# Performance work log

Hardware: AMD Instinct MI355X
Metric: run time of the kernel (lower is better)

The kernel has to match this reference:

```python
import jax, jax.numpy as jnp
import numpy as np

B, N, D, E, H = 4, 2048, 512, 16, 1024
CAP = max(4, min(N, int(N * 2.0 / E)))   # eval capacity_factor = 2.0 -> 256
EPS = 1e-9
THRESH = 0.2  # second_threshold_eval


def setup_inputs() -> dict:
    key = jax.random.key(0)
    ks = jax.random.split(key, 10)
    f32 = jnp.float32
    return {
        "X": jax.random.normal(ks[0], (B, N, D), f32),
        "probs": jax.random.uniform(ks[1], (B, N), f32),
        "W1": jax.random.normal(ks[2], (D, D), f32) * (1.0 / np.sqrt(D)),
        "b1": jnp.zeros((D,), f32),
        "Wg": jax.random.normal(ks[3], (D, E), f32),  # Top2Gating uses randn init
        "We1": jax.random.normal(ks[4], (E, D, H), f32) * (1.0 / np.sqrt(D)),
        "We2": jax.random.normal(ks[5], (E, H, D), f32) * (1.0 / np.sqrt(H)),
        "W3": jax.random.normal(ks[6], (D, 4), f32) * (1.0 / np.sqrt(D)),
        "b3": jnp.zeros((4,), f32),
        "W4": jax.random.normal(ks[7], (4, 1), f32) * 0.5,
        "b4": jnp.zeros((1,), f32),
    }


def top2_gating(x, Wg, probs):
    # x: [B, N, D] -> raw gates [B, N, E]
    raw = jax.nn.softmax(jnp.einsum('bnd,de->bne', x, Wg), axis=-1)
    dt = raw.dtype

    gate1 = jnp.max(raw, axis=-1)
    idx1 = jnp.argmax(raw, axis=-1)
    mask1 = jax.nn.one_hot(idx1, E, dtype=dt)
    density_proxy = raw

    raw_wo1 = raw * (1.0 - mask1)
    gate2 = jnp.max(raw_wo1, axis=-1)
    idx2 = jnp.argmax(raw_wo1, axis=-1)
    mask2 = jax.nn.one_hot(idx2, E, dtype=dt)

    denom = gate1 + gate2 + EPS
    gate1 = gate1 / denom
    gate2 = gate2 / denom

    # load-balancing loss (computed but wrapper discards it)
    density1 = jnp.mean(mask1, axis=-2)
    loss = jnp.mean(jnp.mean(density_proxy, axis=-2) * density1) * float(E ** 2)

    # second policy == 'random'
    mask2 = mask2 * (probs < (gate2 / max(THRESH, EPS))).astype(dt)[..., None]

    # exclusive cumsum along the group dim gives position within each expert
    pos1 = (jnp.cumsum(mask1, axis=-2) - mask1) * mask1          # [B, N, E]
    mask1 = mask1 * (pos1 < float(CAP)).astype(dt)
    mask1_count = jnp.sum(mask1, axis=-2, keepdims=True)
    mask1_flat = jnp.sum(mask1, axis=-1)                          # [B, N]
    pos1_flat = jnp.sum(pos1, axis=-1)
    gate1 = gate1 * mask1_flat

    pos2 = ((jnp.cumsum(mask2, axis=-2) - mask2) + mask1_count) * mask2
    mask2 = mask2 * (pos2 < float(CAP)).astype(dt)
    mask2_flat = jnp.sum(mask2, axis=-1)
    pos2_flat = jnp.sum(pos2, axis=-1)
    gate2 = gate2 * mask2_flat

    # safe one-hot: out-of-range positions map to all-zeros (jax.nn.one_hot semantics)
    oh_p1 = jax.nn.one_hot(pos1_flat.astype(jnp.int32), CAP, dtype=dt)
    oh_p2 = jax.nn.one_hot(pos2_flat.astype(jnp.int32), CAP, dtype=dt)
    oh_e1 = jax.nn.one_hot(idx1, E, dtype=dt)
    oh_e2 = jax.nn.one_hot(idx2, E, dtype=dt)

    combine = ((gate1 * mask1_flat)[..., None, None] * oh_e1[..., :, None] * oh_p1[..., None, :]
               + (gate2 * mask2_flat)[..., None, None] * oh_e2[..., :, None] * oh_p2[..., None, :])
    dispatch = (combine != 0).astype(dt)
    return dispatch, combine, loss


def reference(X, probs, W1, b1, Wg, We1, We2, W3, b3, W4, b4):
    h = X @ W1 + b1                                              # linear1
    dispatch, combine, loss = top2_gating(h, Wg, probs)
    exp_in = jnp.einsum('bnd,bnec->ebcd', h, dispatch)           # dispatch
    hid = jax.nn.leaky_relu(jnp.einsum('ebcd,edh->ebch', exp_in, We1))
    exp_out = jnp.einsum('ebch,ehd->ebcd', hid, We2)             # experts
    moe_out = jnp.einsum('bnec,ebcd->bnd', combine, exp_out)     # combine
    out = (moe_out @ W3 + b3) @ W4 + b4                          # hidden3 -> act3
    return out
```

## Files before the change

kernel.cpp:

```cpp
#include <hip/hip_runtime.h>
#include <hip/hip_bf16.h>

#define NB 4
#define NN 2048
#define ND 512
#define NE 16
#define NH 1024
#define CAP 256
#define NTOK (NB*NN)

typedef __attribute__((ext_vector_type(8))) short bf16x8;
typedef __attribute__((ext_vector_type(4))) float f32x4;
typedef __attribute__((ext_vector_type(8))) unsigned short u16x8;

__device__ __forceinline__ void gload16(const void* gsrc, void* lds) {
    __builtin_amdgcn_global_load_lds((const __attribute__((address_space(1))) void*)gsrc,
                                     (__attribute__((address_space(3))) void*)lds, 16, 0, 0);
}
__device__ __forceinline__ unsigned short f2bf(float f) {
    union { __hip_bfloat16 b; unsigned short u; } v; v.b = __float2bfloat16(f); return v.u;
}

__global__ __launch_bounds__(256) void prep_kernel(const float* __restrict__ W1,
                                                   const float* __restrict__ Wg,
                                                   const float* __restrict__ We1,
                                                   const float* __restrict__ We2,
                                                   const float* __restrict__ W3,
                                                   const float* __restrict__ W4,
                                                   unsigned short* __restrict__ W1B,
                                                   unsigned short* __restrict__ We1B,
                                                   float* __restrict__ WcT,
                                                   float* __restrict__ u,
                                                   float* __restrict__ zbuf) {
    const int tid = threadIdx.x;
    int bid = blockIdx.x;
    if (bid < 512) {
        __shared__ float vvs[ND];
        {
            int d = tid * 2;
            float s0 = 0.f, s1 = 0.f;
            #pragma unroll
            for (int j = 0; j < 4; ++j) {
                s0 += W3[d * 4 + j] * W4[j];
                s1 += W3[(d + 1) * 4 + j] * W4[j];
            }
            vvs[d] = s0; vvs[d + 1] = s1;
        }
        if (bid == 0) zbuf[tid] = 0.f;
        __syncthreads();
        const int w = tid >> 6, l = tid & 63;
        const float4* vv4 = (const float4*)vvs;
        const float4 v0 = vv4[l], v1 = vv4[l + 64];
        float sums[8];
        #pragma unroll
        for (int i = 0; i < 8; ++i) {
            int gr = bid * 32 + w * 8 + i;
            const float4* row = (const float4*)(We2 + (size_t)gr * ND);
            float4 a0 = row[l], a1 = row[l + 64];
            sums[i] = a0.x * v0.x + a0.y * v0.y + a0.z * v0.z + a0.w * v0.w
                    + a1.x * v1.x + a1.y * v1.y + a1.z * v1.z + a1.w * v1.w;
        }
        #pragma unroll
        for (int off = 32; off >= 1; off >>= 1)
            #pragma unroll
            for (int i = 0; i < 8; ++i) sums[i] += __shfl_xor(sums[i], off);
        if (l == 0) {
            int gr0 = bid * 32 + w * 8;
            #pragma unroll
            for (int i = 0; i < 8; ++i) u[gr0 + i] = sums[i];
        }
        return;
    }
    bid -= 512;
    if (bid < 128) {
        const int w = tid >> 6, l = tid & 63;
        const int d = bid * 4 + w;
        float a0 = 0.f, a1 = 0.f, a2 = 0.f, a3 = 0.f, a4 = 0.f, a5 = 0.f, a6 = 0.f, a7 = 0.f;
        float a8 = 0.f, a9 = 0.f, aA = 0.f, aB = 0.f, aC = 0.f, aD = 0.f, aE = 0.f, aF = 0.f;
        #pragma unroll
        for (int ch = 0; ch < 8; ++ch) {
            float x = W1[(size_t)d * ND + ch * 64 + l];
            const float4* wg4 = (const float4*)(Wg + (size_t)(ch * 64 + l) * NE);
            float4 g0 = wg4[0], g1 = wg4[1], g2 = wg4[2], g3 = wg4[3];
            a0 = fmaf(x, g0.x, a0); a1 = fmaf(x, g0.y, a1); a2 = fmaf(x, g0.z, a2); a3 = fmaf(x, g0.w, a3);
            a4 = fmaf(x, g1.x, a4); a5 = fmaf(x, g1.y, a5); a6 = fmaf(x, g1.z, a6); a7 = fmaf(x, g1.w, a7);
            a8 = fmaf(x, g2.x, a8); a9 = fmaf(x, g2.y, a9); aA = fmaf(x, g2.z, aA); aB = fmaf(x, g2.w, aB);
            aC = fmaf(x, g3.x, aC); aD = fmaf(x, g3.y, aD); aE = fmaf(x, g3.z, aE); aF = fmaf(x, g3.w, aF);
        }
        float accs[16] = {a0, a1, a2, a3, a4, a5, a6, a7, a8, a9, aA, aB, aC, aD, aE, aF};
        #pragma unroll
        for (int off = 32; off >= 1; off >>= 1)
            #pragma unroll
            for (int e = 0; e < 16; ++e) accs[e] += __shfl_xor(accs[e], off);
        #pragma unroll
        for (int e = 0; e < 16; ++e)
            if (l == e) WcT[e * ND + d] = accs[e];
        return;
    }
    bid -= 128;
    {
        const float* src; unsigned short* dst; int C; size_t so, dof;
        int d0;
        if (bid < 16) {
            int dblk = bid >> 1, hblk = bid & 1;
            src = W1; C = ND; so = 0;
            d0 = dblk * 64;
            dof = (size_t)(dblk * 512 + hblk * 256) * 64;
            dst = W1B + dof + (size_t)tid * 64;
            src += (size_t)d0 * C + hblk * 256 + tid;
        } else {
            int tb = bid - 16;
            int e = tb >> 5, rem = tb & 31;
            int dblk = rem >> 2, hblk = rem & 3;
            src = We1; C = NH;
            so = (size_t)e * ND * NH;
            d0 = dblk * 64;
            dof = (size_t)((e * 8 + dblk) * NH + hblk * 256) * 64;
            dst = We1B + dof + (size_t)tid * 64;
            src += so + (size_t)d0 * C + hblk * 256 + tid;
        }
        float v[64];
        #pragma unroll
        for (int j = 0; j < 64; ++j) v[j] = src[(size_t)j * C];
        #pragma unroll
        for (int q = 0; q < 8; ++q) {
            u16x8 o;
            #pragma unroll
            for (int j = 0; j < 8; ++j) o[j] = f2bf(v[q * 8 + j]);
            *(u16x8*)(dst + q * 8) = o;
        }
    }
}

__global__ __launch_bounds__(256) void gating_kernel(const float* __restrict__ X,
                                                     const float* __restrict__ WcT,
                                                     const float* __restrict__ probs,
                                                     unsigned short* __restrict__ Xbf,
                                                     int* __restrict__ idx1a, int* __restrict__ idx2a,
                                                     float* __restrict__ g1a, float* __restrict__ g2a,
                                                     int* __restrict__ pos1a, int* __restrict__ pos2a) {
    __shared__ float wc[NE * ND];
    const int tid = threadIdx.x;
    #pragma unroll
    for (int i = 0; i < 32; ++i) wc[tid + 256 * i] = WcT[tid + 256 * i];
    __syncthreads();
    const int w = tid >> 6, l = tid & 63;
    const float4* wc4 = (const float4*)wc;
    for (int j = 0; j < 4; ++j) {
        int tok = blockIdx.x * 16 + j * 4 + w;
        const float4* xrow = (const float4*)(X + (size_t)tok * ND);
        float4 x0 = xrow[l], x1 = xrow[l + 64];
        {
            ushort4 o0, o1;
            o0.x = f2bf(x0.x); o0.y = f2bf(x0.y); o0.z = f2bf(x0.z); o0.w = f2bf(x0.w);
            o1.x = f2bf(x1.x); o1.y = f2bf(x1.y); o1.z = f2bf(x1.z); o1.w = f2bf(x1.w);
            *(ushort4*)(Xbf + (size_t)tok * ND + 4 * l) = o0;
            *(ushort4*)(Xbf + (size_t)tok * ND + 256 + 4 * l) = o1;
        }
        float acc[NE];
        #pragma unroll
        for (int e = 0; e < NE; ++e) {
            float4 w0 = wc4[e * 128 + l], w1 = wc4[e * 128 + l + 64];
            acc[e] = x0.x * w0.x + x0.y * w0.y + x0.z * w0.z + x0.w * w0.w
                   + x1.x * w1.x + x1.y * w1.y + x1.z * w1.z + x1.w * w1.w;
        }
        #pragma unroll
        for (int off = 32; off >= 1; off >>= 1)
            #pragma unroll
            for (int e = 0; e < NE; ++e) acc[e] += __shfl_xor(acc[e], off);

        if (l == 0) {
            float m = acc[0];
            #pragma unroll
            for (int e = 1; e < NE; ++e) m = fmaxf(m, acc[e]);
            float raw[NE]; float s = 0.f;
            #pragma unroll
            for (int e = 0; e < NE; ++e) { raw[e] = expf(acc[e] - m); s += raw[e]; }
            #pragma unroll
            for (int e = 0; e < NE; ++e) raw[e] = raw[e] / s;
            int i1 = 0; float g1 = raw[0];
            #pragma unroll
            for (int e = 1; e < NE; ++e) if (raw[e] > g1) { g1 = raw[e]; i1 = e; }
            int i2 = -1; float g2 = -1.f;
            #pragma unroll
            for (int e = 0; e < NE; ++e) if (e != i1 && raw[e] > g2) { g2 = raw[e]; i2 = e; }
            float denom = g1 + g2 + 1e-9f;
            float g1n = g1 / denom, g2n = g2 / denom;
            bool flag = probs[tok] < (g2n / 0.2f);
            idx1a[tok] = i1;
            idx2a[tok] = flag ? i2 : -1;
            g1a[tok] = g1n;
            g2a[tok] = g2n;
            pos1a[tok] = -1;
            pos2a[tok] = -1;
        }
    }
}

__global__ __launch_bounds__(512) void scan_linear1_kernel(const int* __restrict__ idx1a,
                                                           const int* __restrict__ idx2a,
                                                           int* __restrict__ pos1a, int* __restrict__ pos2a,
                                                           int* __restrict__ slot_token,
                                                           const unsigned short* __restrict__ Xbf,
                                                           const unsigned short* __restrict__ W1B,
                                                           const float* __restrict__ b1,
                                                           unsigned short* __restrict__ hbf) {
    __shared__ char smem[65536];
    const int tid = threadIdx.x;
    const int w = tid >> 6, l = tid & 63;
    if (blockIdx.x < 64) {
        const int bb = blockIdx.x;
        const int b = bb >> 4, e = bb & 15;
        int* cnt1 = (int*)smem;
        int* cnt2 = cnt1 + 8;
        int* slot = slot_token + (e * NB + b) * CAP;
        const unsigned long long below = (l == 0) ? 0ull : ((1ull << l) - 1ull);
        const int base0 = w * 256;
        int c1 = 0, c2 = 0;
        #pragma unroll
        for (int it = 0; it < 4; ++it) {
            int n = base0 + it * 64 + l;
            c1 += __popcll(__ballot(idx1a[b * NN + n] == e));
            c2 += __popcll(__ballot(idx2a[b * NN + n] == e));
        }
        if (l == 0) { cnt1[w] = c1; cnt2[w] = c2; }
        __syncthreads();
        int b1c = 0, t1 = 0, b2c = 0, t2 = 0;
        #pragma unroll
        for (int i = 0; i < 8; ++i) {
            int v1 = cnt1[i], v2 = cnt2[i];
            if (i < w) { b1c += v1; b2c += v2; }
            t1 += v1; t2 += v2;
        }
        const int start2 = (t1 < CAP) ? t1 : CAP;
        int c = b1c;
        #pragma unroll
        for (int it = 0; it < 4; ++it) {
            int n = base0 + it * 64 + l;
            bool p = (idx1a[b * NN + n] == e);
            unsigned long long m = __ballot(p);
            int pre = __popcll(m & below);
            if (p) { int pos = c + pre; if (pos < CAP) { slot[pos] = n; pos1a[b * NN + n] = pos; } }
            c += __popcll(m);
        }
        c = start2 + b2c;
        #pragma unroll
        for (int it = 0; it < 4; ++it) {
            int n = base0 + it * 64 + l;
            bool p = (idx2a[b * NN + n] == e);
            unsigned long long m = __ballot(p);
            int pre = __popcll(m & below);
            if (p) { int pos = c + pre; if (pos < CAP) { slot[pos] = n; pos2a[b * NN + n] = pos; } }
            c += __popcll(m);
        }
        int nfill = start2 + t2; nfill = (nfill < CAP) ? nfill : CAP;
        for (int i = nfill + tid; i < CAP; i += 512) slot[i] = -1;
        return;
    }
    const int lb = blockIdx.x - 64;
    const int m0 = (lb >> 2) * 128, n0 = (lb & 3) * 128;
    const int wm = w >> 1, wn = w & 1;
    const int lr = l & 15, lk = l >> 4;
    char* Ash0 = smem;
    char* Bsh0 = smem + 32768;

    auto stage = [&](int Ks, int buf) {
        #pragma unroll
        for (int i = 0; i < 2; ++i) {
            int o = i * 8192 + tid * 16;
            int r = o >> 7, bb = o & 127;
            int sb = bb ^ ((r & 7) << 4);
            gload16((const char*)Xbf + ((size_t)(m0 + r) * ND + Ks * 64) * 2 + sb,
                    Ash0 + buf * 16384 + i * 8192 + w * 1024);
            gload16((const char*)W1B + ((size_t)(Ks * 512 + n0 + r) * 64) * 2 + sb,
                    Bsh0 + buf * 16384 + i * 8192 + w * 1024);
        }
    };

    f32x4 acc[2][4] = {};
    stage(0, 0);
    __syncthreads();
    for (int Ks = 0; Ks < 8; ++Ks) {
        int buf = Ks & 1;
        if (Ks < 7) stage(Ks + 1, buf ^ 1);
        #pragma unroll
        for (int k32 = 0; k32 < 2; ++k32) {
            int kb = (k32 * 32 + 8 * lk) * 2;
            bf16x8 a[2], bfr[4];
            #pragma unroll
            for (int mi = 0; mi < 2; ++mi) {
                int row = wm * 32 + mi * 16 + lr;
                a[mi] = *(const bf16x8*)(Ash0 + buf * 16384 + row * 128 + (kb ^ ((row & 7) << 4)));
            }
            #pragma unroll
            for (int ni = 0; ni < 4; ++ni) {
                int row = wn * 64 + ni * 16 + lr;
                bfr[ni] = *(const bf16x8*)(Bsh0 + buf * 16384 + row * 128 + (kb ^ ((row & 7) << 4)));
            }
            #pragma unroll
            for (int mi = 0; mi < 2; ++mi)
                #pragma unroll
                for (int ni = 0; ni < 4; ++ni)
                    acc[mi][ni] = __builtin_amdgcn_mfma_f32_16x16x32_bf16(a[mi], bfr[ni], acc[mi][ni], 0, 0, 0);
        }
        __syncthreads();
    }
    #pragma unroll
    for (int mi = 0; mi < 2; ++mi)
        #pragma unroll
        for (int ni = 0; ni < 4; ++ni) {
            int col = n0 + wn * 64 + ni * 16 + lr;
            float bb1 = b1[col];
            #pragma unroll
            for (int r = 0; r < 4; ++r) {
                int m = m0 + wm * 32 + mi * 16 + lk * 4 + r;
                hbf[(size_t)m * ND + col] = f2bf(acc[mi][ni][r] + bb1);
            }
        }
}

__global__ __launch_bounds__(512) void expert_mfma_kernel(const unsigned short* __restrict__ hbf,
                                                          const unsigned short* __restrict__ We1B,
                                                          const float* __restrict__ u,
                                                          const int* __restrict__ slot_token,
                                                          const float* __restrict__ zbuf,
                                                          float* __restrict__ s_slot) {
    __shared__ char Ash[65536];
    __shared__ char Bsh[2][32768];
    __shared__ float u_lds[NH];
    __shared__ float sbuf[8][32];
    __shared__ int toks[64];
    const int tid = threadIdx.x;
    const int w = tid >> 6, l = tid & 63;
    const int wm = w >> 2, wn = w & 3;
    const int lr = l & 15, lk = l >> 4;
    const int bid = blockIdx.x;
    const int e = (bid & 7) | ((bid >> 7) << 3);
    const int chunk = (bid >> 3) & 15;
    const int b = chunk >> 2, c0 = (chunk & 3) * 64;

    if (tid < 64) toks[tid] = slot_token[(e * NB + b) * CAP + c0 + tid];
    u_lds[tid] = u[e * NH + tid];
    u_lds[tid + 512] = u[e * NH + tid + 512];
    __syncthreads();
    #pragma unroll
    for (int i = 0; i < 8; ++i) {
        int r = i * 8 + w;
        int t = toks[r];
        int sb = (l * 16) ^ ((r & 7) << 4);
        const char* src = (t >= 0) ? ((const char*)hbf + ((size_t)(b * NN + t) * ND) * 2 + sb)
                                   : ((const char*)zbuf + sb);
        gload16(src, Ash + i * 8192 + w * 1024);
    }
    auto stageB = [&](int s, int buf) {
        int Hc = s >> 3, Ks = s & 7;
        #pragma unroll
        for (int i = 0; i < 4; ++i) {
            int o = i * 8192 + tid * 16;
            int r = o >> 7, bb = o & 127;
            int sb = bb ^ ((r & 7) << 4);
            gload16((const char*)We1B + (((size_t)(e * 8 + Ks) * NH + Hc * 256 + r) * 64) * 2 + sb,
                    Bsh[buf] + i * 8192 + w * 1024);
        }
    };
    f32x4 acc[2][4] = {};
    float srow[2][4] = {};
    stageB(0, 0);
    __syncthreads();
    for (int s = 0; s < 32; ++s) {
        int buf = s & 1;
        if (s < 31) stageB(s + 1, buf ^ 1);
        #pragma unroll
        for (int k32 = 0; k32 < 2; ++k32) {
            int kbA = ((s & 7) * 64 + k32 * 32 + 8 * lk) * 2;
            int kbB = (k32 * 32 + 8 * lk) * 2;
            bf16x8 a[2], bfr[4];
            #pragma unroll
            for (int mi = 0; mi < 2; ++mi) {
                int row = wm * 32 + mi * 16 + lr;
                a[mi] = *(const bf16x8*)(Ash + row * 1024 + (kbA ^ ((row & 7) << 4)));
            }
            #pragma unroll
            for (int ni = 0; ni < 4; ++ni) {
                int row = wn * 64 + ni * 16 + lr;
                bfr[ni] = *(const bf16x8*)(Bsh[buf] + row * 128 + (kbB ^ ((row & 7) << 4)));
            }
            #pragma unroll
            for (int mi = 0; mi < 2; ++mi)
                #pragma unroll
                for (int ni = 0; ni < 4; ++ni)
                    acc[mi][ni] = __builtin_amdgcn_mfma_f32_16x16x32_bf16(a[mi], bfr[ni], acc[mi][ni], 0, 0, 0);
        }
        if ((s & 7) == 7) {
            int Hc = s >> 3;
            #pragma unroll
            for (int mi = 0; mi < 2; ++mi)
                #pragma unroll
                for (int ni = 0; ni < 4; ++ni) {
                    float uu = u_lds[Hc * 256 + wn * 64 + ni * 16 + lr];
                    #pragma unroll
                    for (int r = 0; r < 4; ++r) {
                        float x = acc[mi][ni][r];
                        x = (x > 0.f) ? x : 0.01f * x;
                        srow[mi][r] = fmaf(x, uu, srow[mi][r]);
                        acc[mi][ni][r] = 0.f;
                    }
                }
        }
        __syncthreads();
    }
    #pragma unroll
    for (int off = 1; off < 16; off <<= 1)
        #pragma unroll
        for (int mi = 0; mi < 2; ++mi)
            #pragma unroll
            for (int r = 0; r < 4; ++r)
                srow[mi][r] += __shfl_xor(srow[mi][r], off);
    if (lr == 0) {
        #pragma unroll
        for (int mi = 0; mi < 2; ++mi)
            #pragma unroll
            for (int r = 0; r < 4; ++r)
                sbuf[w][mi * 16 + lk * 4 + r] = srow[mi][r];
    }
    __syncthreads();
    if (tid < 64) {
        int q = tid >> 5, rl = tid & 31;
        float s = sbuf[q * 4 + 0][rl] + sbuf[q * 4 + 1][rl] + sbuf[q * 4 + 2][rl] + sbuf[q * 4 + 3][rl];
        s_slot[(e * NB + b) * CAP + c0 + tid] = s;
    }
}

__global__ __launch_bounds__(256) void final_kernel(const int* __restrict__ idx1a, const int* __restrict__ idx2a,
                                                    const int* __restrict__ pos1a, const int* __restrict__ pos2a,
                                                    const float* __restrict__ g1a, const float* __restrict__ g2a,
                                                    const float* __restrict__ s_slot,
                                                    const float* __restrict__ b3, const float* __restrict__ W4,
                                                    const float* __restrict__ b4,
                                                    float* __restrict__ out) {
    int tok = blockIdx.x * 256 + threadIdx.x;
    int b = tok >> 11;
    float c0v = 0.f;
    #pragma unroll
    for (int j = 0; j < 4; ++j) c0v += b3[j] * W4[j];
    float s = c0v + b4[0];
    int p1 = pos1a[tok];
    if (p1 >= 0) s += g1a[tok] * s_slot[(idx1a[tok] * NB + b) * CAP + p1];
    int p2 = pos2a[tok];
    if (p2 >= 0) s += g2a[tok] * s_slot[(idx2a[tok] * NB + b) * CAP + p2];
    out[tok] = s;
}

extern "C" void kernel_launch(void* const* d_in, const int* in_sizes, int n_in,
                              void* d_out, int out_size, void* d_ws, size_t ws_size,
                              hipStream_t stream) {
    const float* X    = (const float*)d_in[0];
    const float* probs= (const float*)d_in[1];
    const float* W1   = (const float*)d_in[2];
    const float* b1   = (const float*)d_in[3];
    const float* Wg   = (const float*)d_in[4];
    const float* We1  = (const float*)d_in[5];
    const float* We2  = (const float*)d_in[6];
    const float* W3   = (const float*)d_in[7];
    const float* b3   = (const float*)d_in[8];
    const float* W4   = (const float*)d_in[9];
    const float* b4   = (const float*)d_in[10];
    float* out = (float*)d_out;

    char* ws = (char*)d_ws;
    size_t off = 0;
    auto alloc = [&](size_t bytes) { void* p = ws + off; off += (bytes + 255) & ~(size_t)255; return p; };
    unsigned short* Xbf  = (unsigned short*)alloc((size_t)NTOK * ND * 2);
    unsigned short* hbf  = (unsigned short*)alloc((size_t)NTOK * ND * 2);
    unsigned short* W1B  = (unsigned short*)alloc((size_t)ND * ND * 2);
    unsigned short* We1B = (unsigned short*)alloc((size_t)NE * NH * ND * 2);
    float* WcT     = (float*)alloc(NE * ND * 4);
    float* u       = (float*)alloc(NE * NH * 4);
    float* zbuf    = (float*)alloc(1024);
    int*   idx1a   = (int*)alloc(NTOK * 4);
    int*   idx2a   = (int*)alloc(NTOK * 4);
    int*   pos1a   = (int*)alloc(NTOK * 4);
    int*   pos2a   = (int*)alloc(NTOK * 4);
    float* g1a     = (float*)alloc(NTOK * 4);
    float* g2a     = (float*)alloc(NTOK * 4);
    int*   slot_tok= (int*)alloc(NE * NB * CAP * 4);
    float* s_slot  = (float*)alloc(NE * NB * CAP * 4);
    (void)ws_size; (void)in_sizes; (void)n_in; (void)out_size;

    prep_kernel<<<1168, 256, 0, stream>>>(W1, Wg, We1, We2, W3, W4,
                                          W1B, We1B, WcT, u, zbuf);
    gating_kernel<<<NTOK / 16, 256, 0, stream>>>(X, WcT, probs, Xbf,
                                                 idx1a, idx2a, g1a, g2a, pos1a, pos2a);
    scan_linear1_kernel<<<64 + 256, 512, 0, stream>>>(idx1a, idx2a, pos1a, pos2a, slot_tok,
                                                      Xbf, W1B, b1, hbf);
    expert_mfma_kernel<<<256, 512, 0, stream>>>(hbf, We1B, u, slot_tok, zbuf, s_slot);
    final_kernel<<<NTOK / 256, 256, 0, stream>>>(idx1a, idx2a, pos1a, pos2a, g1a, g2a, s_slot, b3, W4, b4, out);
}
```

Measured before the change: 90.06 us.

## Move We1 bf16 conversion and We2 projection into scan/linear1 kernel

The expert-weight preprocessing (converting We1 to bf16 tiles and projecting We2 onto W3·W4 into u) moves out of the prep kernel and into extra blocks of the scan_linear1 kernel, now sized at 512 threads per block. The prep kernel keeps only the W1 conversion and the Wc fold, so it shrinks and gating can start sooner. The expert-weight work, which does not depend on gating, now runs alongside the scan and linear1 GEMM, hiding its memory traffic on the critical path. The risk is that the extra blocks compete with the GEMM blocks for CUs and bandwidth.

```diff
diff --git a/kernel.cpp b/kernel.cpp
--- a/kernel.cpp
+++ b/kernel.cpp
@@ -23,55 +23,11 @@
 
 __global__ __launch_bounds__(256) void prep_kernel(const float* __restrict__ W1,
                                                    const float* __restrict__ Wg,
-                                                   const float* __restrict__ We1,
-                                                   const float* __restrict__ We2,
-                                                   const float* __restrict__ W3,
-                                                   const float* __restrict__ W4,
                                                    unsigned short* __restrict__ W1B,
-                                                   unsigned short* __restrict__ We1B,
                                                    float* __restrict__ WcT,
-                                                   float* __restrict__ u,
                                                    float* __restrict__ zbuf) {
     const int tid = threadIdx.x;
     int bid = blockIdx.x;
-    if (bid < 512) {
-        __shared__ float vvs[ND];
-        {
-            int d = tid * 2;
-            float s0 = 0.f, s1 = 0.f;
-            #pragma unroll
-            for (int j = 0; j < 4; ++j) {
-                s0 += W3[d * 4 + j] * W4[j];
-                s1 += W3[(d + 1) * 4 + j] * W4[j];
-            }
-            vvs[d] = s0; vvs[d + 1] = s1;
-        }
-        if (bid == 0) zbuf[tid] = 0.f;
-        __syncthreads();
-        const int w = tid >> 6, l = tid & 63;
-        const float4* vv4 = (const float4*)vvs;
-        const float4 v0 = vv4[l], v1 = vv4[l + 64];
-        float sums[8];
-        #pragma unroll
-        for (int i = 0; i < 8; ++i) {
-            int gr = bid * 32 + w * 8 + i;
-            const float4* row = (const float4*)(We2 + (size_t)gr * ND);
-            float4 a0 = row[l], a1 = row[l + 64];
-            sums[i] = a0.x * v0.x + a0.y * v0.y + a0.z * v0.z + a0.w * v0.w
-                    + a1.x * v1.x + a1.y * v1.y + a1.z * v1.z + a1.w * v1.w;
-        }
-        #pragma unroll
-        for (int off = 32; off >= 1; off >>= 1)
-            #pragma unroll
-            for (int i = 0; i < 8; ++i) sums[i] += __shfl_xor(sums[i], off);
-        if (l == 0) {
-            int gr0 = bid * 32 + w * 8;
-            #pragma unroll
-            for (int i = 0; i < 8; ++i) u[gr0 + i] = sums[i];
-        }
-        return;
-    }
-    bid -= 512;
     if (bid < 128) {
         const int w = tid >> 6, l = tid & 63;
         const int d = bid * 4 + w;
@@ -99,29 +55,13 @@
     }
     bid -= 128;
     {
-        const float* src; unsigned short* dst; int C; size_t so, dof;
-        int d0;
-        if (bid < 16) {
-            int dblk = bid >> 1, hblk = bid & 1;
-            src = W1; C = ND; so = 0;
-            d0 = dblk * 64;
-            dof = (size_t)(dblk * 512 + hblk * 256) * 64;
-            dst = W1B + dof + (size_t)tid * 64;
-            src += (size_t)d0 * C + hblk * 256 + tid;
-        } else {
-            int tb = bid - 16;
-            int e = tb >> 5, rem = tb & 31;
-            int dblk = rem >> 2, hblk = rem & 3;
-            src = We1; C = NH;
-            so = (size_t)e * ND * NH;
-            d0 = dblk * 64;
-            dof = (size_t)((e * 8 + dblk) * NH + hblk * 256) * 64;
-            dst = We1B + dof + (size_t)tid * 64;
-            src += so + (size_t)d0 * C + hblk * 256 + tid;
-        }
+        if (bid == 0) zbuf[tid] = 0.f;
+        int dblk = bid >> 1, hblk = bid & 1;
+        const float* src = W1 + (size_t)(dblk * 64) * ND + hblk * 256 + tid;
+        unsigned short* dst = W1B + (size_t)(dblk * 512 + hblk * 256 + tid) * 64;
         float v[64];
         #pragma unroll
-        for (int j = 0; j < 64; ++j) v[j] = src[(size_t)j * C];
+        for (int j = 0; j < 64; ++j) v[j] = src[(size_t)j * ND];
         #pragma unroll
         for (int q = 0; q < 8; ++q) {
             u16x8 o;
@@ -204,7 +144,13 @@
                                                            const unsigned short* __restrict__ Xbf,
                                                            const unsigned short* __restrict__ W1B,
                                                            const float* __restrict__ b1,
-                                                           unsigned short* __restrict__ hbf) {
+                                                           unsigned short* __restrict__ hbf,
+                                                           const float* __restrict__ We1,
+                                                           unsigned short* __restrict__ We1B,
+                                                           const float* __restrict__ We2,
+                                                           const float* __restrict__ W3,
+                                                           const float* __restrict__ W4,
+                                                           float* __restrict__ u) {
     __shared__ char smem[65536];
     const int tid = threadIdx.x;
     const int w = tid >> 6, l = tid & 63;
@@ -257,66 +203,119 @@
         for (int i = nfill + tid; i < CAP; i += 512) slot[i] = -1;
         return;
     }
-    const int lb = blockIdx.x - 64;
-    const int m0 = (lb >> 2) * 128, n0 = (lb & 3) * 128;
-    const int wm = w >> 1, wn = w & 1;
-    const int lr = l & 15, lk = l >> 4;
-    char* Ash0 = smem;
-    char* Bsh0 = smem + 32768;
-
-    auto stage = [&](int Ks, int buf) {
-        #pragma unroll
-        for (int i = 0; i < 2; ++i) {
-            int o = i * 8192 + tid * 16;
-            int r = o >> 7, bb = o & 127;
-            int sb = bb ^ ((r & 7) << 4);
-            gload16((const char*)Xbf + ((size_t)(m0 + r) * ND + Ks * 64) * 2 + sb,
-                    Ash0 + buf * 16384 + i * 8192 + w * 1024);
-            gload16((const char*)W1B + ((size_t)(Ks * 512 + n0 + r) * 64) * 2 + sb,
-                    Bsh0 + buf * 16384 + i * 8192 + w * 1024);
-        }
-    };
-
-    f32x4 acc[2][4] = {};
-    stage(0, 0);
-    __syncthreads();
-    for (int Ks = 0; Ks < 8; ++Ks) {
-        int buf = Ks & 1;
-        if (Ks < 7) stage(Ks + 1, buf ^ 1);
-        #pragma unroll
-        for (int k32 = 0; k32 < 2; ++k32) {
-            int kb = (k32 * 32 + 8 * lk) * 2;
-            bf16x8 a[2], bfr[4];
-            #pragma unroll
-            for (int mi = 0; mi < 2; ++mi) {
-                int row = wm * 32 + mi * 16 + lr;
-                a[mi] = *(const bf16x8*)(Ash0 + buf * 16384 + row * 128 + (kb ^ ((row & 7) << 4)));
+    if (blockIdx.x < 320) {
+        const int lb = blockIdx.x - 64;
+        const int m0 = (lb >> 2) * 128, n0 = (lb & 3) * 128;
+        const int wm = w >> 1, wn = w & 1;
+        const int lr = l & 15, lk = l >> 4;
+        char* Ash0 = smem;
+        char* Bsh0 = smem + 32768;
+
+        auto stage = [&](int Ks, int buf) {
+            #pragma unroll
+            for (int i = 0; i < 2; ++i) {
+                int o = i * 8192 + tid * 16;
+                int r = o >> 7, bb = o & 127;
+                int sb = bb ^ ((r & 7) << 4);
+                gload16((const char*)Xbf + ((size_t)(m0 + r) * ND + Ks * 64) * 2 + sb,
+                        Ash0 + buf * 16384 + i * 8192 + w * 1024);
+                gload16((const char*)W1B + ((size_t)(Ks * 512 + n0 + r) * 64) * 2 + sb,
+                        Bsh0 + buf * 16384 + i * 8192 + w * 1024);
             }
+        };
+
+        f32x4 acc[2][4] = {};
+        stage(0, 0);
+        __syncthreads();
+        for (int Ks = 0; Ks < 8; ++Ks) {
+            int buf = Ks & 1;
+            if (Ks < 7) stage(Ks + 1, buf ^ 1);
+            #pragma unroll
+            for (int k32 = 0; k32 < 2; ++k32) {
+                int kb = (k32 * 32 + 8 * lk) * 2;
+                bf16x8 a[2], bfr[4];
+                #pragma unroll
+                for (int mi = 0; mi < 2; ++mi) {
+                    int row = wm * 32 + mi * 16 + lr;
+                    a[mi] = *(const bf16x8*)(Ash0 + buf * 16384 + row * 128 + (kb ^ ((row & 7) << 4)));
+                }
+                #pragma unroll
+                for (int ni = 0; ni < 4; ++ni) {
+                    int row = wn * 64 + ni * 16 + lr;
+                    bfr[ni] = *(const bf16x8*)(Bsh0 + buf * 16384 + row * 128 + (kb ^ ((row & 7) << 4)));
+                }
+                #pragma unroll
+                for (int mi = 0; mi < 2; ++mi)
+                    #pragma unroll
+                    for (int ni = 0; ni < 4; ++ni)
+                        acc[mi][ni] = __builtin_amdgcn_mfma_f32_16x16x32_bf16(a[mi], bfr[ni], acc[mi][ni], 0, 0, 0);
+            }
+            __syncthreads();
+        }
+        #pragma unroll
+        for (int mi = 0; mi < 2; ++mi)
             #pragma unroll
             for (int ni = 0; ni < 4; ++ni) {
-                int row = wn * 64 + ni * 16 + lr;
-                bfr[ni] = *(const bf16x8*)(Bsh0 + buf * 16384 + row * 128 + (kb ^ ((row & 7) << 4)));
+                int col = n0 + wn * 64 + ni * 16 + lr;
+                float bb1 = b1[col];
+                #pragma unroll
+                for (int r = 0; r < 4; ++r) {
+                    int m = m0 + wm * 32 + mi * 16 + lk * 4 + r;
+                    hbf[(size_t)m * ND + col] = f2bf(acc[mi][ni][r] + bb1);
+                }
             }
-            #pragma unroll
-            for (int mi = 0; mi < 2; ++mi)
-                #pragma unroll
-                for (int ni = 0; ni < 4; ++ni)
-                    acc[mi][ni] = __builtin_amdgcn_mfma_f32_16x16x32_bf16(a[mi], bfr[ni], acc[mi][ni], 0, 0, 0);
+        return;
+    }
+    if (blockIdx.x < 576) {
+        const int tb = blockIdx.x - 320;
+        const int e = tb >> 4, rem = tb & 15;
+        const int dblk = rem >> 1, hblk2 = rem & 1;
+        const float* src = We1 + (size_t)e * ND * NH + (size_t)(dblk * 64) * NH + hblk2 * 512 + tid;
+        unsigned short* dst = We1B + ((size_t)(e * 8 + dblk) * NH + hblk2 * 512 + tid) * 64;
+        float v[64];
+        #pragma unroll
+        for (int j = 0; j < 64; ++j) v[j] = src[(size_t)j * NH];
+        #pragma unroll
+        for (int q = 0; q < 8; ++q) {
+            u16x8 o;
+            #pragma unroll
+            for (int j = 0; j < 8; ++j) o[j] = f2bf(v[q * 8 + j]);
+            *(u16x8*)(dst + q * 8) = o;
+        }
+        return;
+    }
+    {
+        const int ub = blockIdx.x - 576;
+        float* vvs = (float*)smem;
+        {
+            int d = tid;
+            float s0 = 0.f;
+            #pragma unroll
+            for (int j = 0; j < 4; ++j) s0 += W3[d * 4 + j] * W4[j];
+            vvs[d] = s0;
         }
         __syncthreads();
-    }
-    #pragma unroll
-    for (int mi = 0; mi < 2; ++mi)
-        #pragma unroll
-        for (int ni = 0; ni < 4; ++ni) {
-            int col = n0 + wn * 64 + ni * 16 + lr;
-            float bb1 = b1[col];
-            #pragma unroll
-            for (int r = 0; r < 4; ++r) {
-                int m = m0 + wm * 32 + mi * 16 + lk * 4 + r;
-                hbf[(size_t)m * ND + col] = f2bf(acc[mi][ni][r] + bb1);
-            }
-        }
+        const float4* vv4 = (const float4*)vvs;
+        const float4 v0 = vv4[l], v1 = vv4[l + 64];
+        float sums[8];
+        #pragma unroll
+        for (int i = 0; i < 8; ++i) {
+            int gr = ub * 64 + w * 8 + i;
+            const float4* row = (const float4*)(We2 + (size_t)gr * ND);
+            float4 a0 = row[l], a1 = row[l + 64];
+            sums[i] = a0.x * v0.x + a0.y * v0.y + a0.z * v0.z + a0.w * v0.w
+                    + a1.x * v1.x + a1.y * v1.y + a1.z * v1.z + a1.w * v1.w;
+        }
+        #pragma unroll
+        for (int off = 32; off >= 1; off >>= 1)
+            #pragma unroll
+            for (int i = 0; i < 8; ++i) sums[i] += __shfl_xor(sums[i], off);
+        if (l == 0) {
+            int gr0 = ub * 64 + w * 8;
+            #pragma unroll
+            for (int i = 0; i < 8; ++i) u[gr0 + i] = sums[i];
+        }
+    }
 }
 
 __global__ __launch_bounds__(512) void expert_mfma_kernel(const unsigned short* __restrict__ hbf,
@@ -487,12 +486,12 @@
     float* s_slot  = (float*)alloc(NE * NB * CAP * 4);
     (void)ws_size; (void)in_sizes; (void)n_in; (void)out_size;
 
-    prep_kernel<<<1168, 256, 0, stream>>>(W1, Wg, We1, We2, W3, W4,
-                                          W1B, We1B, WcT, u, zbuf);
+    prep_kernel<<<144, 256, 0, stream>>>(W1, Wg, W1B, WcT, zbuf);
     gating_kernel<<<NTOK / 16, 256, 0, stream>>>(X, WcT, probs, Xbf,
                                                  idx1a, idx2a, g1a, g2a, pos1a, pos2a);
-    scan_linear1_kernel<<<64 + 256, 512, 0, stream>>>(idx1a, idx2a, pos1a, pos2a, slot_tok,
-                                                      Xbf, W1B, b1, hbf);
+    scan_linear1_kernel<<<832, 512, 0, stream>>>(idx1a, idx2a, pos1a, pos2a, slot_tok,
+                                                 Xbf, W1B, b1, hbf,
+                                                 We1, We1B, We2, W3, W4, u);
     expert_mfma_kernel<<<256, 512, 0, stream>>>(hbf, We1B, u, slot_tok, zbuf, s_slot);
     final_kernel<<<NTOK / 256, 256, 0, stream>>>(idx1a, idx2a, pos1a, pos2a, g1a, g2a, s_slot, b3, W4, b4, out);
 }
```

After: 90.90 us. Within noise of the previous version (+0.9%).
